# Optimization experiments

Hardware: AMD Instinct MI355X
Metric: run time of the kernel (lower is better)

The kernel has to match this reference:

```python
import jax, jax.numpy as jnp
import numpy as np
from jax import lax

B, N, D = 16, 2048, 256
H = 64  # hidden_dim
EPS = 1e-5


def zero_softmax(x, eps=EPS):
    # zeros stay exactly zero: exp(0)-1 == 0
    e = jnp.exp(x) - 1.0
    return e / (jnp.sum(e, axis=-1, keepdims=True) + eps)


def setup_inputs() -> dict:
    key = jax.random.key(0)
    ks = jax.random.split(key, 9)
    s_in = 1.0 / np.sqrt(D)
    x = jax.random.normal(ks[0], (B, N, D), dtype=jnp.float32)
    Wq = jax.random.uniform(ks[1], (D, H), jnp.float32, -s_in, s_in)
    bq = jax.random.uniform(ks[2], (H,), jnp.float32, -s_in, s_in)
    Wk = jax.random.uniform(ks[3], (D, H), jnp.float32, -s_in, s_in)
    bk = jax.random.uniform(ks[4], (H,), jnp.float32, -s_in, s_in)
    Wv = jax.random.uniform(ks[5], (D, H), jnp.float32, -s_in, s_in)
    bv = jax.random.uniform(ks[6], (H,), jnp.float32, -s_in, s_in)
    s_c = 1.0 / 3.0  # conv fan_in = 1*3*3 = 9
    conv_w = jax.random.uniform(ks[7], (1, 1, 3, 3), jnp.float32, -s_c, s_c)
    conv_b = jax.random.uniform(ks[8], (1,), jnp.float32, -s_c, s_c)
    return {"x": x, "Wq": Wq, "bq": bq, "Wk": Wk, "bk": bk,
            "Wv": Wv, "bv": bv, "conv_w": conv_w, "conv_b": conv_b}


def reference(x, Wq, bq, Wk, bk, Wv, bv, conv_w, conv_b):
    scale = H ** (-0.5)
    q = jnp.einsum('bnd,dh->bnh', x, Wq) + bq
    k = jnp.einsum('bnd,dh->bnh', x, Wk) + bk
    v = jnp.einsum('bnd,dh->bnh', x, Wv) + bv
    A_dense = jnp.einsum('bnh,bmh->bnm', q, k) * scale  # [B, N, N]
    A_in = A_dense[:, None, :, :]  # [B, 1, N, N]
    A_conv = lax.conv_general_dilated(
        A_in, conv_w, window_strides=(1, 1), padding='SAME',
        dimension_numbers=('NCHW', 'OIHW', 'NCHW')) + conv_b[None, :, None, None]
    A_conv = jax.nn.sigmoid(A_conv)[:, 0, :, :]
    A_sparse = jax.nn.relu(A_dense - A_conv)
    A_norm = zero_softmax(A_sparse)
    return jnp.einsum('bnm,bmh->bnh', A_norm, v)
```

## Files before the change

kernel.cpp:

```cpp
#include <hip/hip_runtime.h>
#include <hip/hip_bf16.h>

typedef __bf16 bf16_t;
typedef __bf16 bf16x8 __attribute__((ext_vector_type(8)));
typedef float  floatx4 __attribute__((ext_vector_type(4)));

#define BQ 16
#define NTOK 2048
#define DIM 256
#define HD 64

__global__ __launch_bounds__(256) void k_prep(const float* __restrict__ Wq,
                                              const float* __restrict__ Wk,
                                              const float* __restrict__ Wv,
                                              bf16_t* __restrict__ wt,
                                              float* __restrict__ outz,
                                              float* __restrict__ rsz) {
    int o = blockIdx.x * 256 + threadIdx.x;
    if (o < 49152) {
        int w = o >> 14;
        int r = o & 16383;
        int h = r >> 8;
        int d = r & 255;
        const float* W = (w == 0) ? Wq : ((w == 1) ? Wk : Wv);
        wt[o] = (bf16_t)W[d * 64 + h];
    }
    float4 z = make_float4(0.f, 0.f, 0.f, 0.f);
    for (int u = o; u < 532480; u += 262144) {
        if (u < 524288) ((float4*)outz)[u] = z;
        else            ((float4*)rsz)[u - 524288] = z;
    }
}

#define XS 264
__global__ __launch_bounds__(256) void k_qkv(const float* __restrict__ x,
                                             const bf16_t* __restrict__ wt,
                                             const float* __restrict__ bq,
                                             const float* __restrict__ bk,
                                             const float* __restrict__ bv,
                                             bf16_t* __restrict__ qb,
                                             bf16_t* __restrict__ kb,
                                             bf16_t* __restrict__ vt) {
    __shared__ bf16_t x_ls[64 * XS];
    __shared__ bf16_t vt_ls[64 * 72];

    int b  = blockIdx.x >> 5;
    int t0 = (blockIdx.x & 31) << 6;
    int t  = threadIdx.x;
    int lane = t & 63;
    int w    = t >> 6;
    int m_   = lane & 15;
    int q4   = lane >> 4;

    for (int tau = t; tau < 4096; tau += 256) {
        int row = tau >> 6, ch = tau & 63;
        float4 v = ((const float4*)x)[(size_t)(b * NTOK + t0 + row) * 64 + ch];
        bf16_t tmp[4] = {(bf16_t)v.x, (bf16_t)v.y, (bf16_t)v.z, (bf16_t)v.w};
        *(uint2*)(&x_ls[row * XS + ch * 4]) = *(uint2*)tmp;
    }
    __syncthreads();

    for (int wi = 0; wi < 3; ++wi) {
        const bf16_t* wtw = wt + wi * 16384;
        floatx4 acc[4];
        #pragma unroll
        for (int mt = 0; mt < 4; ++mt) acc[mt] = floatx4{0.f, 0.f, 0.f, 0.f};

        #pragma unroll
        for (int ks = 0; ks < 8; ++ks) {
            bf16x8 bfrag = *(const bf16x8*)(wtw + (16 * w + m_) * 256 + ks * 32 + q4 * 8);
            #pragma unroll
            for (int mt = 0; mt < 4; ++mt) {
                bf16x8 afrag = *(const bf16x8*)(&x_ls[(16 * mt + m_) * XS + ks * 32 + q4 * 8]);
                acc[mt] = __builtin_amdgcn_mfma_f32_16x16x32_bf16(afrag, bfrag, acc[mt], 0, 0, 0);
            }
        }
        const float* bias_p = (wi == 0) ? bq : ((wi == 1) ? bk : bv);
        float bias = bias_p[16 * w + m_];
        float scale = (wi == 0) ? 0.125f : 1.0f;

        if (wi < 2) {
            bf16_t* dst = (wi == 0) ? qb : kb;
            #pragma unroll
            for (int mt = 0; mt < 4; ++mt)
                #pragma unroll
                for (int r = 0; r < 4; ++r) {
                    int tok = t0 + 16 * mt + 4 * q4 + r;
                    dst[(size_t)(b * NTOK + tok) * 64 + 16 * w + m_] = (bf16_t)((acc[mt][r] + bias) * scale);
                }
        } else {
            #pragma unroll
            for (int mt = 0; mt < 4; ++mt)
                #pragma unroll
                for (int r = 0; r < 4; ++r)
                    vt_ls[(16 * w + m_) * 72 + 16 * mt + 4 * q4 + r] = (bf16_t)(acc[mt][r] + bias);
            __syncthreads();
            for (int tau = t; tau < 512; tau += 256) {
                int h = tau >> 3, ch = tau & 7;
                uint4 val = *(const uint4*)(&vt_ls[h * 72 + ch * 8]);
                *(uint4*)(vt + (size_t)(b * 64 + h) * NTOK + t0 + ch * 8) = val;
            }
        }
    }
}

#define SA 68
#define SP 72
#define RINT 62
#define L2E 1.44269504f

static __device__ __forceinline__ bf16x8 as_bf16x8(uint4 u) {
    union { uint4 a; bf16x8 b; } c; c.a = u; return c.b;
}

__global__ __launch_bounds__(512) void k_attn(const bf16_t* __restrict__ qb,
                                              const bf16_t* __restrict__ kb,
                                              const bf16_t* __restrict__ vt,
                                              const float* __restrict__ conv_w,
                                              const float* __restrict__ conv_b,
                                              float* __restrict__ outp,
                                              float* __restrict__ rsg) {
    __shared__ bf16_t k_ls[2][64 * SP];
    __shared__ bf16_t v_ls[64 * SP];
    __shared__ bf16_t p_ls[64 * SP];
    __shared__ float  A_ls[64 * SA];

    int b  = blockIdx.z;
    int r0 = blockIdx.x * RINT;
    int cy = blockIdx.y;
    int it_beg = (cy * 34) / 3;
    int it_end = ((cy + 1) * 34) / 3;

    int t = threadIdx.x, lane = t & 63, w = t >> 6;
    int m_ = lane & 15, q4 = lane >> 4;
    int wtj = w & 3;
    int wti = (w >> 2) << 1;

    const uint* vt32 = (const uint*)vt + (size_t)b * 64 * 1024;
    const bf16_t* kb_b = kb + (size_t)b * NTOK * 64;

    int krow = t >> 3, kch = t & 7;

    uint4 kreg;
    uint  vreg[4];

    auto load_k = [&](int c0) {
        int g = c0 - 1 + krow;
        uint4 val = make_uint4(0u, 0u, 0u, 0u);
        if (g >= 0 && g < NTOK)
            val = *(const uint4*)(kb_b + (size_t)g * 64 + kch * 8);
        kreg = val;
    };
    auto load_v = [&](int c0) {
        int cb2 = (c0 >> 1) + 4 * kch;
        #pragma unroll
        for (int j = 0; j < 4; ++j) {
            uint val = 0u;
            if (cb2 + j < 1024) val = vt32[krow * 1024 + cb2 + j];
            vreg[j] = val;
        }
    };

    load_k(it_beg * RINT);
    load_v(it_beg * RINT);

    float cw[9];
    #pragma unroll
    for (int i = 0; i < 9; ++i) cw[i] = conv_w[i] * L2E;
    float cbv = conv_b[0] * L2E;

    bf16x8 qreg[2][2];
    #pragma unroll
    for (int p = 0; p < 2; ++p) {
        int g = r0 - 1 + 16 * (wti + p) + m_;
        #pragma unroll
        for (int ks = 0; ks < 2; ++ks) {
            uint4 val = make_uint4(0u, 0u, 0u, 0u);
            if (g >= 0 && g < NTOK)
                val = *(const uint4*)(qb + (size_t)(b * NTOK + g) * 64 + ks * 32 + q4 * 8);
            qreg[p][ks] = as_bf16x8(val);
        }
    }

    for (int u = t; u < 2304; u += 512) ((uint*)p_ls)[u] = 0u;
    if (t < 256) A_ls[(t >> 2) * SA + 64 + (t & 3)] = 0.f;

    *(uint4*)(&k_ls[0][krow * SP + kch * 8]) = kreg;
    load_k((it_beg + 1) * RINT);

    floatx4 accO[2];
    accO[0] = floatx4{0.f, 0.f, 0.f, 0.f};
    accO[1] = floatx4{0.f, 0.f, 0.f, 0.f};
    float rs[2] = {0.f, 0.f};

    int u2 = t >> 4;
    int gq = t & 15;
    bool gq15 = (gq == 15);
    int ci = 2 * u2 + 1;
    const float* cbase = &A_ls[(ci - 1) * SA + 4 * gq];

    __syncthreads();

    for (int itg = it_beg; itg < it_end; ++itg) {
        int rel = (itg - it_beg) & 1;
        const bf16_t* kcur = k_ls[rel];

        {
            bf16x8 bfr0 = *(const bf16x8*)(&kcur[(16 * wtj + m_) * SP + q4 * 8]);
            bf16x8 bfr1 = *(const bf16x8*)(&kcur[(16 * wtj + m_) * SP + 32 + q4 * 8]);
            #pragma unroll
            for (int p = 0; p < 2; ++p) {
                floatx4 a = floatx4{0.f, 0.f, 0.f, 0.f};
                a = __builtin_amdgcn_mfma_f32_16x16x32_bf16(qreg[p][0], bfr0, a, 0, 0, 0);
                a = __builtin_amdgcn_mfma_f32_16x16x32_bf16(qreg[p][1], bfr1, a, 0, 0, 0);
                int rbase = 16 * (wti + p) + 4 * q4;
                #pragma unroll
                for (int r = 0; r < 4; ++r)
                    A_ls[(rbase + r) * SA + 16 * wtj + m_] = a[r];
            }
        }
        __syncthreads();

        *(uint4*)(&k_ls[rel ^ 1][krow * SP + kch * 8]) = kreg;
        *(uint4*)(&v_ls[krow * SP + 8 * kch]) = make_uint4(vreg[0], vreg[1], vreg[2], vreg[3]);
        load_k((itg + 2) * RINT);
        load_v((itg + 1) * RINT);

        if (u2 < 31) {
            float a0[6], a1[6], a2[6], a3[6];
            *(float4*)(a0)     = *(const float4*)(cbase);
            *(float2*)(a0 + 4) = *(const float2*)(cbase + 4);
            *(float4*)(a1)     = *(const float4*)(cbase + SA);
            *(float2*)(a1 + 4) = *(const float2*)(cbase + SA + 4);
            *(float4*)(a2)     = *(const float4*)(cbase + 2 * SA);
            *(float2*)(a2 + 4) = *(const float2*)(cbase + 2 * SA + 4);
            *(float4*)(a3)     = *(const float4*)(cbase + 3 * SA);
            *(float2*)(a3 + 4) = *(const float2*)(cbase + 3 * SA + 4);
            float es0 = 0.f, es1 = 0.f;
            bf16_t q0[4], q1[4];
            #pragma unroll
            for (int x = 0; x < 4; ++x) {
                float c0v = cbv
                    + cw[0] * a0[x] + cw[1] * a0[x + 1] + cw[2] * a0[x + 2]
                    + cw[3] * a1[x] + cw[4] * a1[x + 1] + cw[5] * a1[x + 2]
                    + cw[6] * a2[x] + cw[7] * a2[x + 1] + cw[8] * a2[x + 2];
                float c1v = cbv
                    + cw[0] * a1[x] + cw[1] * a1[x + 1] + cw[2] * a1[x + 2]
                    + cw[3] * a2[x] + cw[4] * a2[x + 1] + cw[5] * a2[x + 2]
                    + cw[6] * a3[x] + cw[7] * a3[x + 1] + cw[8] * a3[x + 2];
                float sig0 = __builtin_amdgcn_rcpf(1.f + __builtin_amdgcn_exp2f(-c0v));
                float sig1 = __builtin_amdgcn_rcpf(1.f + __builtin_amdgcn_exp2f(-c1v));
                float s0 = fmaxf(a1[x + 1] - sig0, 0.f);
                float s1 = fmaxf(a2[x + 1] - sig1, 0.f);
                float e0 = __builtin_amdgcn_exp2f(s0 * L2E) - 1.f;
                float e1 = __builtin_amdgcn_exp2f(s1 * L2E) - 1.f;
                if (x >= 2) { e0 = gq15 ? 0.f : e0; e1 = gq15 ? 0.f : e1; }
                q0[x] = (bf16_t)e0; q1[x] = (bf16_t)e1;
                es0 += e0; es1 += e1;
            }
            rs[0] += es0; rs[1] += es1;
            *(uint2*)(&p_ls[ci * SP + 4 * gq])       = *(uint2*)q0;
            *(uint2*)(&p_ls[(ci + 1) * SP + 4 * gq]) = *(uint2*)q1;
        }
        __syncthreads();

        #pragma unroll
        for (int ks = 0; ks < 2; ++ks) {
            bf16x8 bfr = *(const bf16x8*)(&v_ls[(16 * wtj + m_) * SP + ks * 32 + q4 * 8]);
            #pragma unroll
            for (int p = 0; p < 2; ++p) {
                bf16x8 af = *(const bf16x8*)(&p_ls[(16 * (wti + p) + m_) * SP + ks * 32 + q4 * 8]);
                accO[p] = __builtin_amdgcn_mfma_f32_16x16x32_bf16(af, bfr, accO[p], 0, 0, 0);
            }
        }
    }

    float s0 = rs[0], s1 = rs[1];
    #pragma unroll
    for (int d = 1; d < 16; d <<= 1) {
        s0 += __shfl_xor(s0, d);
        s1 += __shfl_xor(s1, d);
    }
    if ((t & 15) == 0 && u2 < 31) {
        int gr = r0 + 2 * u2;
        if (gr < NTOK)     atomicAdd(&rsg[b * NTOK + gr],     s0);
        if (gr + 1 < NTOK) atomicAdd(&rsg[b * NTOK + gr + 1], s1);
    }

    #pragma unroll
    for (int p = 0; p < 2; ++p) {
        int rbase = 16 * (wti + p) + 4 * q4;
        #pragma unroll
        for (int r = 0; r < 4; ++r) {
            int i = rbase + r;
            int grow = r0 + i - 1;
            if (i >= 1 && i < 63 && grow < NTOK)
                atomicAdd(&outp[((size_t)(b * NTOK + grow) << 6) + 16 * wtj + m_], accO[p][r]);
        }
    }
}

__global__ __launch_bounds__(256) void k_norm(float* __restrict__ out,
                                              const float* __restrict__ rsg) {
    int gid = blockIdx.x * 256 + threadIdx.x;
    float4 o = ((float4*)out)[gid];
    float d = rsg[gid >> 4] + 1e-5f;
    float inv = 1.f / d;
    o.x *= inv; o.y *= inv; o.z *= inv; o.w *= inv;
    ((float4*)out)[gid] = o;
}

extern "C" void kernel_launch(void* const* d_in, const int* in_sizes, int n_in,
                              void* d_out, int out_size, void* d_ws, size_t ws_size,
                              hipStream_t stream) {
    const float* x  = (const float*)d_in[0];
    const float* Wq = (const float*)d_in[1];
    const float* bq = (const float*)d_in[2];
    const float* Wk = (const float*)d_in[3];
    const float* bk = (const float*)d_in[4];
    const float* Wv = (const float*)d_in[5];
    const float* bv = (const float*)d_in[6];
    const float* cw = (const float*)d_in[7];
    const float* cb = (const float*)d_in[8];
    float* out = (float*)d_out;

    char* ws = (char*)d_ws;
    bf16_t* wt = (bf16_t*)ws;
    bf16_t* qb = (bf16_t*)(ws + 98304);
    bf16_t* kb = (bf16_t*)(ws + 98304 + 4194304);
    bf16_t* vt = (bf16_t*)(ws + 98304 + 8388608);
    float*  rsg = (float*)(ws + 98304 + 12582912);

    k_prep<<<dim3(1024), dim3(256), 0, stream>>>(Wq, Wk, Wv, wt, out, rsg);
    k_qkv<<<dim3(512), dim3(256), 0, stream>>>(x, wt, bq, bk, bv, qb, kb, vt);
    k_attn<<<dim3(34, 3, BQ), dim3(512), 0, stream>>>(qb, kb, vt, cw, cb, out, rsg);
    k_norm<<<dim3(2048), dim3(256), 0, stream>>>(out, rsg);
}
```

Before: 201.9 us.

## Compute 3x3 conv via MFMA on bf16 scores and drop K double buffer

Measured after the change: 203.5 us. Within noise of the previous version (+0.8%).

```diff
diff --git a/kernel.cpp b/kernel.cpp
--- a/kernel.cpp
+++ b/kernel.cpp
@@ -104,7 +104,6 @@
     }
 }
 
-#define SA 68
 #define SP 72
 #define RINT 62
 #define L2E 1.44269504f
@@ -113,17 +112,18 @@
     union { uint4 a; bf16x8 b; } c; c.a = u; return c.b;
 }
 
-__global__ __launch_bounds__(512) void k_attn(const bf16_t* __restrict__ qb,
-                                              const bf16_t* __restrict__ kb,
-                                              const bf16_t* __restrict__ vt,
-                                              const float* __restrict__ conv_w,
-                                              const float* __restrict__ conv_b,
-                                              float* __restrict__ outp,
-                                              float* __restrict__ rsg) {
-    __shared__ bf16_t k_ls[2][64 * SP];
+__global__ __launch_bounds__(512, 3) void k_attn(const bf16_t* __restrict__ qb,
+                                                 const bf16_t* __restrict__ kb,
+                                                 const bf16_t* __restrict__ vt,
+                                                 const float* __restrict__ conv_w,
+                                                 const float* __restrict__ conv_b,
+                                                 float* __restrict__ outp,
+                                                 float* __restrict__ rsg) {
+    __shared__ bf16_t k_ls[64 * SP];
     __shared__ bf16_t v_ls[64 * SP];
-    __shared__ bf16_t p_ls[64 * SP];
-    __shared__ float  A_ls[64 * SA];
+    __shared__ bf16_t a_bf[64 * SP];
+    __shared__ bf16_t p_raw[64 * SP + 8];
+    bf16_t* pv_ls = p_raw + 8;
 
     int b  = blockIdx.z;
     int r0 = blockIdx.x * RINT;
@@ -143,7 +143,6 @@
 
     uint4 kreg;
     uint  vreg[4];
-
     auto load_k = [&](int c0) {
         int g = c0 - 1 + krow;
         uint4 val = make_uint4(0u, 0u, 0u, 0u);
@@ -164,10 +163,22 @@
     load_k(it_beg * RINT);
     load_v(it_beg * RINT);
 
-    float cw[9];
-    #pragma unroll
-    for (int i = 0; i < 9; ++i) cw[i] = conv_w[i] * L2E;
-    float cbv = conv_b[0] * L2E;
+    float cw9[9];
+    #pragma unroll
+    for (int i = 0; i < 9; ++i) cw9[i] = conv_w[i] * L2E;
+    float cbv2 = conv_b[0] * L2E;
+    int koff = ((wtj & 1) << 3) + ((wtj & 2) * 12);
+    bf16x8 bK[3];
+    #pragma unroll
+    for (int di = 0; di < 3; ++di) {
+        bf16_t tmp[8];
+        #pragma unroll
+        for (int jj = 0; jj < 8; ++jj) {
+            int d = koff + q4 * 8 + jj - (16 * wtj + m_) + 1;
+            tmp[jj] = (bf16_t)((d >= 0 && d < 3) ? cw9[3 * di + d] : 0.f);
+        }
+        bK[di] = *(bf16x8*)tmp;
+    }
 
     bf16x8 qreg[2][2];
     #pragma unroll
@@ -182,85 +193,66 @@
         }
     }
 
-    for (int u = t; u < 2304; u += 512) ((uint*)p_ls)[u] = 0u;
-    if (t < 256) A_ls[(t >> 2) * SA + 64 + (t & 3)] = 0.f;
-
-    *(uint4*)(&k_ls[0][krow * SP + kch * 8]) = kreg;
+    for (int u = t; u < 2308; u += 512) ((uint*)p_raw)[u] = 0u;
+
+    *(uint4*)(&k_ls[krow * SP + kch * 8]) = kreg;
     load_k((it_beg + 1) * RINT);
 
-    floatx4 accO[2];
+    floatx4 accO[2], rsacc[2];
     accO[0] = floatx4{0.f, 0.f, 0.f, 0.f};
     accO[1] = floatx4{0.f, 0.f, 0.f, 0.f};
-    float rs[2] = {0.f, 0.f};
-
-    int u2 = t >> 4;
-    int gq = t & 15;
-    bool gq15 = (gq == 15);
-    int ci = 2 * u2 + 1;
-    const float* cbase = &A_ls[(ci - 1) * SA + 4 * gq];
+    rsacc[0] = floatx4{0.f, 0.f, 0.f, 0.f};
+    rsacc[1] = floatx4{0.f, 0.f, 0.f, 0.f};
+
+    float mj = ((wtj == 0 && m_ == 0) || (wtj == 3 && m_ == 15)) ? 0.f : 1.f;
+    int jm1 = 16 * wtj + m_ - 1;
 
     __syncthreads();
 
     for (int itg = it_beg; itg < it_end; ++itg) {
-        int rel = (itg - it_beg) & 1;
-        const bf16_t* kcur = k_ls[rel];
-
+        floatx4 areg[2];
         {
-            bf16x8 bfr0 = *(const bf16x8*)(&kcur[(16 * wtj + m_) * SP + q4 * 8]);
-            bf16x8 bfr1 = *(const bf16x8*)(&kcur[(16 * wtj + m_) * SP + 32 + q4 * 8]);
+            bf16x8 bfr0 = *(const bf16x8*)(&k_ls[(16 * wtj + m_) * SP + q4 * 8]);
+            bf16x8 bfr1 = *(const bf16x8*)(&k_ls[(16 * wtj + m_) * SP + 32 + q4 * 8]);
             #pragma unroll
             for (int p = 0; p < 2; ++p) {
                 floatx4 a = floatx4{0.f, 0.f, 0.f, 0.f};
                 a = __builtin_amdgcn_mfma_f32_16x16x32_bf16(qreg[p][0], bfr0, a, 0, 0, 0);
                 a = __builtin_amdgcn_mfma_f32_16x16x32_bf16(qreg[p][1], bfr1, a, 0, 0, 0);
+                areg[p] = a;
                 int rbase = 16 * (wti + p) + 4 * q4;
                 #pragma unroll
                 for (int r = 0; r < 4; ++r)
-                    A_ls[(rbase + r) * SA + 16 * wtj + m_] = a[r];
+                    a_bf[(rbase + r) * SP + 16 * wtj + m_] = (bf16_t)a[r];
             }
         }
         __syncthreads();
 
-        *(uint4*)(&k_ls[rel ^ 1][krow * SP + kch * 8]) = kreg;
+        *(uint4*)(&k_ls[krow * SP + kch * 8]) = kreg;
         *(uint4*)(&v_ls[krow * SP + 8 * kch]) = make_uint4(vreg[0], vreg[1], vreg[2], vreg[3]);
         load_k((itg + 2) * RINT);
         load_v((itg + 1) * RINT);
 
-        if (u2 < 31) {
-            float a0[6], a1[6], a2[6], a3[6];
-            *(float4*)(a0)     = *(const float4*)(cbase);
-            *(float2*)(a0 + 4) = *(const float2*)(cbase + 4);
-            *(float4*)(a1)     = *(const float4*)(cbase + SA);
-            *(float2*)(a1 + 4) = *(const float2*)(cbase + SA + 4);
-            *(float4*)(a2)     = *(const float4*)(cbase + 2 * SA);
-            *(float2*)(a2 + 4) = *(const float2*)(cbase + 2 * SA + 4);
-            *(float4*)(a3)     = *(const float4*)(cbase + 3 * SA);
-            *(float2*)(a3 + 4) = *(const float2*)(cbase + 3 * SA + 4);
-            float es0 = 0.f, es1 = 0.f;
-            bf16_t q0[4], q1[4];
-            #pragma unroll
-            for (int x = 0; x < 4; ++x) {
-                float c0v = cbv
-                    + cw[0] * a0[x] + cw[1] * a0[x + 1] + cw[2] * a0[x + 2]
-                    + cw[3] * a1[x] + cw[4] * a1[x + 1] + cw[5] * a1[x + 2]
-                    + cw[6] * a2[x] + cw[7] * a2[x + 1] + cw[8] * a2[x + 2];
-                float c1v = cbv
-                    + cw[0] * a1[x] + cw[1] * a1[x + 1] + cw[2] * a1[x + 2]
-                    + cw[3] * a2[x] + cw[4] * a2[x + 1] + cw[5] * a2[x + 2]
-                    + cw[6] * a3[x] + cw[7] * a3[x + 1] + cw[8] * a3[x + 2];
-                float sig0 = __builtin_amdgcn_rcpf(1.f + __builtin_amdgcn_exp2f(-c0v));
-                float sig1 = __builtin_amdgcn_rcpf(1.f + __builtin_amdgcn_exp2f(-c1v));
-                float s0 = fmaxf(a1[x + 1] - sig0, 0.f);
-                float s1 = fmaxf(a2[x + 1] - sig1, 0.f);
-                float e0 = __builtin_amdgcn_exp2f(s0 * L2E) - 1.f;
-                float e1 = __builtin_amdgcn_exp2f(s1 * L2E) - 1.f;
-                if (x >= 2) { e0 = gq15 ? 0.f : e0; e1 = gq15 ? 0.f : e1; }
-                q0[x] = (bf16_t)e0; q1[x] = (bf16_t)e1;
-                es0 += e0; es1 += e1;
-            }
-            rs[0] += es0; rs[1] += es1;
-            *(uint2*)(&p_ls[ci * SP + 4 * gq])       = *(uint2*)q0;
-            *(uint2*)(&p_ls[(ci + 1) * SP + 4 * gq]) = *(uint2*)q1;
+        #pragma unroll
+        for (int p = 0; p < 2; ++p) {
+            int arow = 16 * (wti + p) + m_ - 1;
+            floatx4 c = floatx4{cbv2, cbv2, cbv2, cbv2};
+            #pragma unroll
+            for (int di = 0; di < 3; ++di) {
+                bf16x8 af = *(const bf16x8*)(&a_bf[((arow + di) & 63) * SP + koff + q4 * 8]);
+                c = __builtin_amdgcn_mfma_f32_16x16x32_bf16(af, bK[di], c, 0, 0, 0);
+            }
+            int rbase = 16 * (wti + p) + 4 * q4;
+            #pragma unroll
+            for (int r = 0; r < 4; ++r) {
+                float sig = __builtin_amdgcn_rcpf(1.f + __builtin_amdgcn_exp2f(-c[r]));
+                float s = fmaxf(areg[p][r] - sig, 0.f);
+                float ev = (__builtin_amdgcn_exp2f(s * L2E) - 1.f) * mj;
+                if (p == 0 && r == 0) { if (wti == 0) ev = (q4 == 0) ? 0.f : ev; }
+                if (p == 1 && r == 3) { if (wti == 2) ev = (q4 == 3) ? 0.f : ev; }
+                rsacc[p][r] += ev;
+                pv_ls[(rbase + r) * SP + jm1] = (bf16_t)ev;
+            }
         }
         __syncthreads();
 
@@ -269,23 +261,26 @@
             bf16x8 bfr = *(const bf16x8*)(&v_ls[(16 * wtj + m_) * SP + ks * 32 + q4 * 8]);
             #pragma unroll
             for (int p = 0; p < 2; ++p) {
-                bf16x8 af = *(const bf16x8*)(&p_ls[(16 * (wti + p) + m_) * SP + ks * 32 + q4 * 8]);
+                bf16x8 af = *(const bf16x8*)(&pv_ls[(16 * (wti + p) + m_) * SP + ks * 32 + q4 * 8]);
                 accO[p] = __builtin_amdgcn_mfma_f32_16x16x32_bf16(af, bfr, accO[p], 0, 0, 0);
             }
         }
     }
 
-    float s0 = rs[0], s1 = rs[1];
-    #pragma unroll
-    for (int d = 1; d < 16; d <<= 1) {
-        s0 += __shfl_xor(s0, d);
-        s1 += __shfl_xor(s1, d);
-    }
-    if ((t & 15) == 0 && u2 < 31) {
-        int gr = r0 + 2 * u2;
-        if (gr < NTOK)     atomicAdd(&rsg[b * NTOK + gr],     s0);
-        if (gr + 1 < NTOK) atomicAdd(&rsg[b * NTOK + gr + 1], s1);
-    }
+    #pragma unroll
+    for (int p = 0; p < 2; ++p)
+        #pragma unroll
+        for (int r = 0; r < 4; ++r) {
+            float s = rsacc[p][r];
+            s += __shfl_xor(s, 1);
+            s += __shfl_xor(s, 2);
+            s += __shfl_xor(s, 4);
+            s += __shfl_xor(s, 8);
+            if (m_ == 0) {
+                int grow = r0 + 16 * (wti + p) + 4 * q4 + r - 1;
+                if ((unsigned)grow < NTOK) atomicAdd(&rsg[b * NTOK + grow], s);
+            }
+        }
 
     #pragma unroll
     for (int p = 0; p < 2; ++p) {
```
